# Kernel optimization log

Hardware: AMD Instinct MI355X
Metric: run time of the kernel (lower is better)

The kernel has to match this reference:

```python
import jax, jax.numpy as jnp
import numpy as np

B, N, D, A, E, T, H, O = 2, 2048, 64, 16, 2, 5, 128, 1


def setup_inputs() -> dict:
    key = jax.random.key(0)
    ks = jax.random.split(key, 12)
    s = 0.02  # torch init: normal(0, 0.02), biases zero
    return {
        "prop_state": jax.random.normal(ks[0], (B, N, D), jnp.float32),
        "annotation": jax.random.normal(ks[1], (B, N, A), jnp.float32),
        "adj_mat": jax.random.uniform(ks[2], (B, N, 2 * N * E), jnp.float32),
        "W_in": s * jax.random.normal(ks[3], (E, D, D), jnp.float32),
        "b_in": jnp.zeros((E, D), jnp.float32),
        "W_out": s * jax.random.normal(ks[4], (E, D, D), jnp.float32),
        "b_out": jnp.zeros((E, D), jnp.float32),
        "Wr": s * jax.random.normal(ks[5], (3 * D, D), jnp.float32),
        "br": jnp.zeros((D,), jnp.float32),
        "Wz": s * jax.random.normal(ks[6], (3 * D, D), jnp.float32),
        "bz": jnp.zeros((D,), jnp.float32),
        "Wh": s * jax.random.normal(ks[7], (3 * D, D), jnp.float32),
        "bh": jnp.zeros((D,), jnp.float32),
        "Wo1": s * jax.random.normal(ks[8], (D + A, H), jnp.float32),
        "bo1": jnp.zeros((H,), jnp.float32),
        "Wo2": s * jax.random.normal(ks[9], (H, O), jnp.float32),
        "bo2": jnp.zeros((O,), jnp.float32),
    }


def reference(prop_state, annotation, adj_mat, W_in, b_in, W_out, b_out,
              Wr, br, Wz, bz, Wh, bh, Wo1, bo1, Wo2, bo2):
    Bb, Nn, Dd = prop_state.shape
    Ee = W_in.shape[0]
    A_in = adj_mat[:, :, : Nn * Ee]   # [B, N, E*N]
    A_out = adj_mat[:, :, Nn * Ee :]  # [B, N, E*N]
    h = prop_state
    for _ in range(T):
        # per-edge-type linear maps; edge-type-major flatten (index = e*N + v)
        ins = (jnp.einsum('bnd,edk->benk', h, W_in) + b_in[None, :, None, :]).reshape(Bb, Ee * Nn, Dd)
        outs = (jnp.einsum('bnd,edk->benk', h, W_out) + b_out[None, :, None, :]).reshape(Bb, Ee * Nn, Dd)
        a_in = jnp.einsum('bnm,bmd->bnd', A_in, ins)
        a_out = jnp.einsum('bnm,bmd->bnd', A_out, outs)
        a = jnp.concatenate([a_in, a_out, h], axis=-1)          # [B, N, 3D]
        r = jax.nn.sigmoid(a @ Wr + br)
        z = jax.nn.sigmoid(a @ Wz + bz)
        joint = jnp.concatenate([a_in, a_out, r * h], axis=-1)  # [B, N, 3D]
        h_hat = jnp.tanh(joint @ Wh + bh)
        h = (1.0 - z) * h + z * h_hat
    x = jnp.concatenate([h, annotation], axis=-1)               # [B, N, D+A]
    x = jax.nn.sigmoid(x @ Wo1 + bo1)
    x = x @ Wo2 + bo2                                           # [B, N, O]
    return x.sum(axis=2)                                        # [B, N]
```

## Files before the change

kernel.cpp:

```cpp
#include <hip/hip_runtime.h>
#include <cstdint>
#include <cstddef>

#define B_ 2
#define N_ 2048
#define D_ 64
#define E_ 2
#define T_ 5

typedef short bf16x8 __attribute__((ext_vector_type(8)));
typedef unsigned short u16x8 __attribute__((ext_vector_type(8)));
typedef float f32x16 __attribute__((ext_vector_type(16)));

__device__ __forceinline__ unsigned short f2bf(float f) {
    unsigned int x = __float_as_uint(f);
    x += 0x7FFFu + ((x >> 16) & 1u);
    return (unsigned short)(x >> 16);
}

__global__ void convert_kernel(const float* __restrict__ adj, u16x8* __restrict__ Abf) {
    int rt = blockIdx.x, c = blockIdx.y, bd = blockIdx.z;
    int b = bd >> 1, dir = bd & 1;
    int tid = threadIdx.x;

    __shared__ __align__(16) unsigned short sb[32][520];

    const float* base = adj + ((size_t)(b * N_ + rt * 32)) * (2 * N_ * E_) + dir * (N_ * E_) + c * 512;

    #pragma unroll
    for (int p = 0; p < 4; ++p) {
        int r = p * 8 + (tid >> 5);
        int i = tid & 31;
        const float* rowp = base + (size_t)r * (2 * N_ * E_);
        #pragma unroll
        for (int j = 0; j < 4; ++j) {
            float4 f = *(const float4*)(rowp + i * 4 + j * 128);
            int kl = i * 4 + j * 128;
            sb[r][kl + 0] = f2bf(f.x);
            sb[r][kl + 1] = f2bf(f.y);
            sb[r][kl + 2] = f2bf(f.z);
            sb[r][kl + 3] = f2bf(f.w);
        }
    }
    __syncthreads();

    int l = tid & 63;
    int row = l & 31, khalf = l >> 5;
    int ktl0 = tid >> 6;
    u16x8* dst = Abf + ((size_t)(bd * 64 + rt) * 256 + c * 32 + ktl0) * 64 + l;
    #pragma unroll
    for (int q = 0; q < 8; ++q) {
        int ktl = ktl0 + q * 4;
        u16x8 v = *(const u16x8*)&sb[row][ktl * 16 + khalf * 8];
        dst[(size_t)q * 4 * 64] = v;
    }
}

__global__ void transform_kernel(const float* __restrict__ h,
                                 const float* __restrict__ W_in, const float* __restrict__ b_in,
                                 const float* __restrict__ W_out, const float* __restrict__ b_out,
                                 u16x8* __restrict__ VT) {
    int y = blockIdx.y;
    int e = y & 1, dir = (y >> 1) & 1, b = y >> 2;
    int bd = y >> 1;
    const float* W = (dir ? W_out : W_in) + e * D_ * D_;
    const float* bias = (dir ? b_out : b_in) + e * D_;
    int n0 = blockIdx.x * 64;

    __shared__ float hs[64][65];
    __shared__ float Ws[64][64];
    __shared__ float os[64][65];

    int tid = threadIdx.x;
    #pragma unroll
    for (int i = 0; i < 16; ++i) {
        int idx = tid + 256 * i;
        int r = idx >> 6, c = idx & 63;
        hs[r][c] = h[((size_t)(b * N_ + n0 + r)) * D_ + c];
        Ws[r][c] = W[idx];
    }
    __syncthreads();

    int g = tid >> 6, l = tid & 63;
    float acc[16];
    #pragma unroll
    for (int j = 0; j < 16; ++j) acc[j] = bias[g * 16 + j];
    for (int k = 0; k < 64; ++k) {
        float hv = hs[l][k];
        #pragma unroll
        for (int j = 0; j < 16; ++j) acc[j] = fmaf(hv, Ws[k][g * 16 + j], acc[j]);
    }
    #pragma unroll
    for (int j = 0; j < 16; ++j) os[l][g * 16 + j] = acc[j];
    __syncthreads();

    #pragma unroll
    for (int c = 0; c < 2; ++c) {
        int chunk = tid + 256 * c;
        int kt_local = chunk >> 7;
        int sub = (chunk >> 6) & 1;
        int ln = chunk & 63;
        int d = sub * 32 + (ln & 31);
        int nbase = kt_local * 16 + (ln >> 5) * 8;
        u16x8 o;
        #pragma unroll
        for (int j = 0; j < 8; ++j) o[j] = f2bf(os[nbase + j][d]);
        int ktg = e * 128 + blockIdx.x * 4 + kt_local;
        VT[((size_t)bd * 512 + ktg * 2 + sub) * 64 + ln] = o;
    }
}

__global__ void __launch_bounds__(512, 2) aggregate_kernel(
        const bf16x8* __restrict__ Abf, const bf16x8* __restrict__ VT,
        float* __restrict__ apart) {
    int bx = blockIdx.x;
    int bd = blockIdx.y;
    int sp = blockIdx.z;
    int tid = threadIdx.x;
    int w = tid >> 6, lane = tid & 63;
    int rt = bx * 8 + w;
    int kt0 = sp * 32;

    const bf16x8* Ap = Abf + ((size_t)(bd * 64 + rt) * 256 + kt0) * 64 + lane;
    const bf16x8* Vp = VT + (size_t)bd * 32768 + (size_t)kt0 * 128 + lane;

    f32x16 acc0 = {}, acc1 = {};
    #pragma unroll 4
    for (int kk = 0; kk < 32; ++kk) {
        bf16x8 a  = Ap[(size_t)kk * 64];
        bf16x8 b0 = Vp[(size_t)kk * 128];
        bf16x8 b1 = Vp[(size_t)kk * 128 + 64];
        acc0 = __builtin_amdgcn_mfma_f32_32x32x16_bf16(a, b0, acc0, 0, 0, 0);
        acc1 = __builtin_amdgcn_mfma_f32_32x32x16_bf16(a, b1, acc1, 0, 0, 0);
    }

    float* Cp = apart + ((size_t)(sp * 4 + bd) * 2048) * 64;
    int col = lane & 31;
    int rbase = rt * 32 + 4 * (lane >> 5);
    #pragma unroll
    for (int reg = 0; reg < 16; ++reg) {
        int row = rbase + (reg & 3) + 8 * (reg >> 2);
        Cp[(size_t)row * 64 + col]      = acc0[reg];
        Cp[(size_t)row * 64 + col + 32] = acc1[reg];
    }
}

__global__ void gru_kernel(float* __restrict__ h,
                           const float* __restrict__ apart,
                           const float* __restrict__ Wr, const float* __restrict__ br,
                           const float* __restrict__ Wz, const float* __restrict__ bz,
                           const float* __restrict__ Wh, const float* __restrict__ bh) {
    int tid = threadIdx.x;
    int grp = tid >> 6, d = tid & 63;
    int g = blockIdx.x * 16 + grp;
    int b = g >> 11, n = g & 2047;

    __shared__ float sa[16][3][64];
    float ain = 0.f, aout = 0.f;
    #pragma unroll
    for (int s = 0; s < 8; ++s) {
        ain  += apart[(((size_t)(s * 4 + b * 2    )) * 2048 + n) * 64 + d];
        aout += apart[(((size_t)(s * 4 + b * 2 + 1)) * 2048 + n) * 64 + d];
    }
    float h_d = h[(size_t)g * 64 + d];
    sa[grp][0][d] = ain;
    sa[grp][1][d] = aout;
    sa[grp][2][d] = h_d;
    __syncthreads();

    float accr = br[d], accz = bz[d];
    #pragma unroll 8
    for (int k = 0; k < 64; ++k) {
        float a0 = sa[grp][0][k], a1 = sa[grp][1][k], a2 = sa[grp][2][k];
        accr = fmaf(a0, Wr[k * 64 + d], accr);
        accr = fmaf(a1, Wr[(64 + k) * 64 + d], accr);
        accr = fmaf(a2, Wr[(128 + k) * 64 + d], accr);
        accz = fmaf(a0, Wz[k * 64 + d], accz);
        accz = fmaf(a1, Wz[(64 + k) * 64 + d], accz);
        accz = fmaf(a2, Wz[(128 + k) * 64 + d], accz);
    }
    float r = 1.0f / (1.0f + expf(-accr));
    float z = 1.0f / (1.0f + expf(-accz));

    __syncthreads();
    sa[grp][2][d] = r * h_d;
    __syncthreads();

    float acch = bh[d];
    #pragma unroll 8
    for (int k = 0; k < 64; ++k) {
        float a0 = sa[grp][0][k], a1 = sa[grp][1][k], a2 = sa[grp][2][k];
        acch = fmaf(a0, Wh[k * 64 + d], acch);
        acch = fmaf(a1, Wh[(64 + k) * 64 + d], acch);
        acch = fmaf(a2, Wh[(128 + k) * 64 + d], acch);
    }
    float hh = tanhf(acch);
    h[(size_t)g * 64 + d] = (1.0f - z) * h_d + z * hh;
}

__global__ void output_kernel(const float* __restrict__ h, const float* __restrict__ ann,
                              const float* __restrict__ Wo1, const float* __restrict__ bo1,
                              const float* __restrict__ Wo2, const float* __restrict__ bo2,
                              float* __restrict__ out) {
    int tid = threadIdx.x;
    int grp = tid >> 7, j = tid & 127;
    int g = blockIdx.x * 2 + grp;

    __shared__ float sx[2][80];
    __shared__ float sy[2][128];
    if (j < 64)       sx[grp][j] = h[(size_t)g * 64 + j];
    else if (j < 80)  sx[grp][j] = ann[(size_t)g * 16 + (j - 64)];
    __syncthreads();

    float acc = bo1[j];
    #pragma unroll
    for (int i = 0; i < 80; ++i) acc = fmaf(sx[grp][i], Wo1[i * 128 + j], acc);
    float y = 1.0f / (1.0f + expf(-acc));
    sy[grp][j] = y * Wo2[j];
    __syncthreads();

    if (j == 0) {
        float s = bo2[0];
        #pragma unroll
        for (int k = 0; k < 128; ++k) s += sy[grp][k];
        out[g] = s;
    }
}

extern "C" void kernel_launch(void* const* d_in, const int* in_sizes, int n_in,
                              void* d_out, int out_size, void* d_ws, size_t ws_size,
                              hipStream_t stream) {
    const float* prop = (const float*)d_in[0];
    const float* ann  = (const float*)d_in[1];
    const float* adj  = (const float*)d_in[2];
    const float* W_in = (const float*)d_in[3];
    const float* b_in = (const float*)d_in[4];
    const float* W_out= (const float*)d_in[5];
    const float* b_out= (const float*)d_in[6];
    const float* Wr   = (const float*)d_in[7];
    const float* br   = (const float*)d_in[8];
    const float* Wz   = (const float*)d_in[9];
    const float* bz   = (const float*)d_in[10];
    const float* Wh   = (const float*)d_in[11];
    const float* bh   = (const float*)d_in[12];
    const float* Wo1  = (const float*)d_in[13];
    const float* bo1  = (const float*)d_in[14];
    const float* Wo2  = (const float*)d_in[15];
    const float* bo2  = (const float*)d_in[16];
    float* out = (float*)d_out;

    char* ws = (char*)d_ws;
    u16x8* Abf   = (u16x8*)ws;
    u16x8* VT    = (u16x8*)(ws + (64ull << 20));
    float* apart = (float*)(ws + (66ull << 20));
    float* h     = (float*)(ws + (82ull << 20));

    convert_kernel<<<dim3(64, 8, 4), 256, 0, stream>>>(adj, Abf);
    hipMemcpyAsync(h, prop, (size_t)B_ * N_ * D_ * sizeof(float),
                   hipMemcpyDeviceToDevice, stream);

    for (int t = 0; t < T_; ++t) {
        transform_kernel<<<dim3(32, 8), 256, 0, stream>>>(
            h, W_in, b_in, W_out, b_out, VT);
        aggregate_kernel<<<dim3(8, 4, 8), 512, 0, stream>>>(
            (const bf16x8*)Abf, (const bf16x8*)VT, apart);
        gru_kernel<<<dim3(B_ * N_ / 16), 1024, 0, stream>>>(
            h, apart, Wr, br, Wz, bz, Wh, bh);
    }
    output_kernel<<<dim3(B_ * N_ / 2), 256, 0, stream>>>(
        h, ann, Wo1, bo1, Wo2, bo2, out);
}
```

Baseline: 483.0 us.

## Fuse timestep loop into one persistent cooperative kernel with grid syncs

Replaces the per-timestep transform, aggregate, GRU and output kernel launches with a single cooperative kernel of 256 workgroups that runs all phases and separates them with grid.sync(). Each workgroup keeps its 16 rows of hidden state in shared memory across timesteps, so h no longer round-trips through global memory and the initial device-to-device copy is dropped. This removes about 16 kernel launches and their tail gaps. In exchange it pays grid-wide barrier costs, and the GRU and transform phases now use fewer threads per row.

```diff
diff --git a/kernel.cpp b/kernel.cpp
--- a/kernel.cpp
+++ b/kernel.cpp
@@ -1,6 +1,9 @@
 #include <hip/hip_runtime.h>
+#include <hip/hip_cooperative_groups.h>
 #include <cstdint>
 #include <cstddef>
+
+namespace cg = cooperative_groups;
 
 #define B_ 2
 #define N_ 2048
@@ -56,71 +59,55 @@
     }
 }
 
-__global__ void transform_kernel(const float* __restrict__ h,
-                                 const float* __restrict__ W_in, const float* __restrict__ b_in,
-                                 const float* __restrict__ W_out, const float* __restrict__ b_out,
-                                 u16x8* __restrict__ VT) {
-    int y = blockIdx.y;
-    int e = y & 1, dir = (y >> 1) & 1, b = y >> 2;
-    int bd = y >> 1;
-    const float* W = (dir ? W_out : W_in) + e * D_ * D_;
+struct SM {
+    float hs[16][64];
+    float os[4][16][66];
+    float sa[16][3][64];
+    float red[4][2];
+};
+
+__device__ __forceinline__ void transform_emit(
+        SM* sm, u16x8* VT,
+        const float* W_in, const float* b_in,
+        const float* W_out, const float* b_out,
+        int b, int ktgl, int tid)
+{
+    int u = tid >> 6, lane = tid & 63;
+    int dir = u & 1, e = (u >> 1) & 1, nh = u >> 2;
+    const float* W    = (dir ? W_out : W_in) + e * D_ * D_;
     const float* bias = (dir ? b_out : b_in) + e * D_;
-    int n0 = blockIdx.x * 64;
-
-    __shared__ float hs[64][65];
-    __shared__ float Ws[64][64];
-    __shared__ float os[64][65];
-
-    int tid = threadIdx.x;
-    #pragma unroll
-    for (int i = 0; i < 16; ++i) {
-        int idx = tid + 256 * i;
-        int r = idx >> 6, c = idx & 63;
-        hs[r][c] = h[((size_t)(b * N_ + n0 + r)) * D_ + c];
-        Ws[r][c] = W[idx];
-    }
-    __syncthreads();
-
-    int g = tid >> 6, l = tid & 63;
-    float acc[16];
-    #pragma unroll
-    for (int j = 0; j < 16; ++j) acc[j] = bias[g * 16 + j];
+    int d = lane;
+    float acc[8];
+    #pragma unroll
+    for (int i = 0; i < 8; ++i) acc[i] = bias[d];
     for (int k = 0; k < 64; ++k) {
-        float hv = hs[l][k];
-        #pragma unroll
-        for (int j = 0; j < 16; ++j) acc[j] = fmaf(hv, Ws[k][g * 16 + j], acc[j]);
-    }
-    #pragma unroll
-    for (int j = 0; j < 16; ++j) os[l][g * 16 + j] = acc[j];
-    __syncthreads();
-
-    #pragma unroll
-    for (int c = 0; c < 2; ++c) {
-        int chunk = tid + 256 * c;
-        int kt_local = chunk >> 7;
-        int sub = (chunk >> 6) & 1;
-        int ln = chunk & 63;
-        int d = sub * 32 + (ln & 31);
-        int nbase = kt_local * 16 + (ln >> 5) * 8;
-        u16x8 o;
-        #pragma unroll
-        for (int j = 0; j < 8; ++j) o[j] = f2bf(os[nbase + j][d]);
-        int ktg = e * 128 + blockIdx.x * 4 + kt_local;
-        VT[((size_t)bd * 512 + ktg * 2 + sub) * 64 + ln] = o;
-    }
-}
-
-__global__ void __launch_bounds__(512, 2) aggregate_kernel(
-        const bf16x8* __restrict__ Abf, const bf16x8* __restrict__ VT,
-        float* __restrict__ apart) {
-    int bx = blockIdx.x;
-    int bd = blockIdx.y;
-    int sp = blockIdx.z;
-    int tid = threadIdx.x;
+        float wv = W[k * 64 + d];
+        #pragma unroll
+        for (int i = 0; i < 8; ++i) acc[i] = fmaf(sm->hs[nh * 8 + i][k], wv, acc[i]);
+    }
+    int de = dir * 2 + e;
+    #pragma unroll
+    for (int i = 0; i < 8; ++i) sm->os[de][nh * 8 + i][d] = acc[i];
+    __syncthreads();
+
+    int sub = u >> 2;
+    int dd = sub * 32 + (lane & 31);
+    int nb = (lane >> 5) * 8;
+    u16x8 o;
+    #pragma unroll
+    for (int j = 0; j < 8; ++j) o[j] = f2bf(sm->os[de][nb + j][dd]);
+    int bd = b * 2 + dir;
+    int ktg = e * 128 + ktgl;
+    VT[((size_t)bd * 512 + ktg * 2 + sub) * 64 + lane] = o;
+}
+
+__device__ __forceinline__ void aggregate_phase(
+        const bf16x8* Abf, const bf16x8* VT, float* apart, int wg, int tid)
+{
+    int rb = wg & 7, bd = (wg >> 3) & 3, sp = wg >> 5;
     int w = tid >> 6, lane = tid & 63;
-    int rt = bx * 8 + w;
+    int rt = rb * 8 + w;
     int kt0 = sp * 32;
-
     const bf16x8* Ap = Abf + ((size_t)(bd * 64 + rt) * 256 + kt0) * 64 + lane;
     const bf16x8* Vp = VT + (size_t)bd * 32768 + (size_t)kt0 * 128 + lane;
 
@@ -133,7 +120,6 @@
         acc0 = __builtin_amdgcn_mfma_f32_32x32x16_bf16(a, b0, acc0, 0, 0, 0);
         acc1 = __builtin_amdgcn_mfma_f32_32x32x16_bf16(a, b1, acc1, 0, 0, 0);
     }
-
     float* Cp = apart + ((size_t)(sp * 4 + bd) * 2048) * 64;
     int col = lane & 31;
     int rbase = rt * 32 + 4 * (lane >> 5);
@@ -145,86 +131,121 @@
     }
 }
 
-__global__ void gru_kernel(float* __restrict__ h,
-                           const float* __restrict__ apart,
-                           const float* __restrict__ Wr, const float* __restrict__ br,
-                           const float* __restrict__ Wz, const float* __restrict__ bz,
-                           const float* __restrict__ Wh, const float* __restrict__ bh) {
-    int tid = threadIdx.x;
-    int grp = tid >> 6, d = tid & 63;
-    int g = blockIdx.x * 16 + grp;
-    int b = g >> 11, n = g & 2047;
-
-    __shared__ float sa[16][3][64];
-    float ain = 0.f, aout = 0.f;
-    #pragma unroll
-    for (int s = 0; s < 8; ++s) {
-        ain  += apart[(((size_t)(s * 4 + b * 2    )) * 2048 + n) * 64 + d];
-        aout += apart[(((size_t)(s * 4 + b * 2 + 1)) * 2048 + n) * 64 + d];
-    }
-    float h_d = h[(size_t)g * 64 + d];
-    sa[grp][0][d] = ain;
-    sa[grp][1][d] = aout;
-    sa[grp][2][d] = h_d;
-    __syncthreads();
-
-    float accr = br[d], accz = bz[d];
-    #pragma unroll 8
-    for (int k = 0; k < 64; ++k) {
-        float a0 = sa[grp][0][k], a1 = sa[grp][1][k], a2 = sa[grp][2][k];
-        accr = fmaf(a0, Wr[k * 64 + d], accr);
-        accr = fmaf(a1, Wr[(64 + k) * 64 + d], accr);
-        accr = fmaf(a2, Wr[(128 + k) * 64 + d], accr);
-        accz = fmaf(a0, Wz[k * 64 + d], accz);
-        accz = fmaf(a1, Wz[(64 + k) * 64 + d], accz);
-        accz = fmaf(a2, Wz[(128 + k) * 64 + d], accz);
-    }
-    float r = 1.0f / (1.0f + expf(-accr));
-    float z = 1.0f / (1.0f + expf(-accz));
-
-    __syncthreads();
-    sa[grp][2][d] = r * h_d;
-    __syncthreads();
-
-    float acch = bh[d];
-    #pragma unroll 8
-    for (int k = 0; k < 64; ++k) {
-        float a0 = sa[grp][0][k], a1 = sa[grp][1][k], a2 = sa[grp][2][k];
-        acch = fmaf(a0, Wh[k * 64 + d], acch);
-        acch = fmaf(a1, Wh[(64 + k) * 64 + d], acch);
-        acch = fmaf(a2, Wh[(128 + k) * 64 + d], acch);
-    }
-    float hh = tanhf(acch);
-    h[(size_t)g * 64 + d] = (1.0f - z) * h_d + z * hh;
-}
-
-__global__ void output_kernel(const float* __restrict__ h, const float* __restrict__ ann,
-                              const float* __restrict__ Wo1, const float* __restrict__ bo1,
-                              const float* __restrict__ Wo2, const float* __restrict__ bo2,
-                              float* __restrict__ out) {
-    int tid = threadIdx.x;
-    int grp = tid >> 7, j = tid & 127;
-    int g = blockIdx.x * 2 + grp;
-
-    __shared__ float sx[2][80];
-    __shared__ float sy[2][128];
-    if (j < 64)       sx[grp][j] = h[(size_t)g * 64 + j];
-    else if (j < 80)  sx[grp][j] = ann[(size_t)g * 16 + (j - 64)];
-    __syncthreads();
-
-    float acc = bo1[j];
-    #pragma unroll
-    for (int i = 0; i < 80; ++i) acc = fmaf(sx[grp][i], Wo1[i * 128 + j], acc);
-    float y = 1.0f / (1.0f + expf(-acc));
-    sy[grp][j] = y * Wo2[j];
-    __syncthreads();
-
-    if (j == 0) {
-        float s = bo2[0];
-        #pragma unroll
-        for (int k = 0; k < 128; ++k) s += sy[grp][k];
-        out[g] = s;
-    }
+__device__ __forceinline__ void gru_phase(
+        SM* sm, const float* apart,
+        const float* Wr, const float* br, const float* Wz, const float* bz,
+        const float* Wh, const float* bh, int b, int n0, int tid)
+{
+    int u = tid >> 6, d = tid & 63;
+    #pragma unroll
+    for (int s = 0; s < 2; ++s) {
+        int nl = u * 2 + s;
+        int n = n0 + nl;
+        float ain = 0.f, aout = 0.f;
+        #pragma unroll
+        for (int sp = 0; sp < 8; ++sp) {
+            ain  += apart[(((size_t)(sp * 4 + b * 2    )) * 2048 + n) * 64 + d];
+            aout += apart[(((size_t)(sp * 4 + b * 2 + 1)) * 2048 + n) * 64 + d];
+        }
+        float h_d = sm->hs[nl][d];
+        sm->sa[nl][0][d] = ain;
+        sm->sa[nl][1][d] = aout;
+        sm->sa[nl][2][d] = h_d;
+        float accr = br[d], accz = bz[d];
+        #pragma unroll 8
+        for (int k = 0; k < 64; ++k) {
+            float a0 = sm->sa[nl][0][k], a1 = sm->sa[nl][1][k], a2 = sm->sa[nl][2][k];
+            accr = fmaf(a0, Wr[k * 64 + d], accr);
+            accr = fmaf(a1, Wr[(64 + k) * 64 + d], accr);
+            accr = fmaf(a2, Wr[(128 + k) * 64 + d], accr);
+            accz = fmaf(a0, Wz[k * 64 + d], accz);
+            accz = fmaf(a1, Wz[(64 + k) * 64 + d], accz);
+            accz = fmaf(a2, Wz[(128 + k) * 64 + d], accz);
+        }
+        float r = 1.0f / (1.0f + expf(-accr));
+        float z = 1.0f / (1.0f + expf(-accz));
+        sm->sa[nl][2][d] = r * h_d;
+        float acch = bh[d];
+        #pragma unroll 8
+        for (int k = 0; k < 64; ++k) {
+            float a0 = sm->sa[nl][0][k], a1 = sm->sa[nl][1][k], a2 = sm->sa[nl][2][k];
+            acch = fmaf(a0, Wh[k * 64 + d], acch);
+            acch = fmaf(a1, Wh[(64 + k) * 64 + d], acch);
+            acch = fmaf(a2, Wh[(128 + k) * 64 + d], acch);
+        }
+        float hh = tanhf(acch);
+        sm->hs[nl][d] = (1.0f - z) * h_d + z * hh;
+    }
+}
+
+__device__ __forceinline__ void output_phase(
+        SM* sm, const float* ann,
+        const float* Wo1, const float* bo1, const float* Wo2, const float* bo2,
+        float* out, int g0, int tid)
+{
+    int sub = tid >> 7, j = tid & 127;
+    int wv = (tid >> 6) & 1;
+    #pragma unroll
+    for (int s = 0; s < 4; ++s) {
+        int nl = sub * 4 + s;
+        int g = g0 + nl;
+        float acc = bo1[j];
+        #pragma unroll
+        for (int i = 0; i < 64; ++i) acc = fmaf(sm->hs[nl][i], Wo1[i * 128 + j], acc);
+        #pragma unroll
+        for (int i = 0; i < 16; ++i) acc = fmaf(ann[(size_t)g * 16 + i], Wo1[(64 + i) * 128 + j], acc);
+        float y = 1.0f / (1.0f + expf(-acc));
+        float v = y * Wo2[j];
+        #pragma unroll
+        for (int off = 32; off > 0; off >>= 1) v += __shfl_down(v, off, 64);
+        if ((tid & 63) == 0) sm->red[sub][wv] = v;
+        __syncthreads();
+        if (j == 0) out[g] = sm->red[sub][0] + sm->red[sub][1] + bo2[0];
+        __syncthreads();
+    }
+}
+
+__global__ void __launch_bounds__(512, 1) ggnn_coop(
+        const float* prop, const float* ann,
+        const bf16x8* Abf, u16x8* VT, float* apart,
+        const float* W_in, const float* b_in,
+        const float* W_out, const float* b_out,
+        const float* Wr, const float* br,
+        const float* Wz, const float* bz,
+        const float* Wh, const float* bh,
+        const float* Wo1, const float* bo1,
+        const float* Wo2, const float* bo2,
+        float* out)
+{
+    cg::grid_group grid = cg::this_grid();
+    __shared__ SM sm;
+    int wg = blockIdx.x, tid = threadIdx.x;
+    int g0 = wg * 16;
+    int b = g0 >> 11;
+    int n0 = g0 & 2047;
+    int ktgl = n0 >> 4;
+
+    #pragma unroll
+    for (int i = 0; i < 2; ++i) {
+        int idx = tid + i * 512;
+        sm.hs[idx >> 6][idx & 63] = prop[(size_t)g0 * 64 + idx];
+    }
+    __syncthreads();
+    transform_emit(&sm, VT, W_in, b_in, W_out, b_out, b, ktgl, tid);
+    grid.sync();
+
+    for (int t = 0; t < T_; ++t) {
+        aggregate_phase(Abf, (const bf16x8*)VT, apart, wg, tid);
+        grid.sync();
+        gru_phase(&sm, apart, Wr, br, Wz, bz, Wh, bh, b, n0, tid);
+        __syncthreads();
+        if (t < T_ - 1) {
+            transform_emit(&sm, VT, W_in, b_in, W_out, b_out, b, ktgl, tid);
+            grid.sync();
+        }
+    }
+    __syncthreads();
+    output_phase(&sm, ann, Wo1, bo1, Wo2, bo2, out, g0, tid);
 }
 
 extern "C" void kernel_launch(void* const* d_in, const int* in_sizes, int n_in,
@@ -250,23 +271,19 @@
     float* out = (float*)d_out;
 
     char* ws = (char*)d_ws;
-    u16x8* Abf   = (u16x8*)ws;
-    u16x8* VT    = (u16x8*)(ws + (64ull << 20));
-    float* apart = (float*)(ws + (66ull << 20));
-    float* h     = (float*)(ws + (82ull << 20));
+    u16x8* Abf    = (u16x8*)ws;
+    u16x8* VT     = (u16x8*)(ws + (64ull << 20));
+    float* apart  = (float*)(ws + (66ull << 20));
 
     convert_kernel<<<dim3(64, 8, 4), 256, 0, stream>>>(adj, Abf);
-    hipMemcpyAsync(h, prop, (size_t)B_ * N_ * D_ * sizeof(float),
-                   hipMemcpyDeviceToDevice, stream);
-
-    for (int t = 0; t < T_; ++t) {
-        transform_kernel<<<dim3(32, 8), 256, 0, stream>>>(
-            h, W_in, b_in, W_out, b_out, VT);
-        aggregate_kernel<<<dim3(8, 4, 8), 512, 0, stream>>>(
-            (const bf16x8*)Abf, (const bf16x8*)VT, apart);
-        gru_kernel<<<dim3(B_ * N_ / 16), 1024, 0, stream>>>(
-            h, apart, Wr, br, Wz, bz, Wh, bh);
-    }
-    output_kernel<<<dim3(B_ * N_ / 2), 256, 0, stream>>>(
-        h, ann, Wo1, bo1, Wo2, bo2, out);
-}
+
+    const bf16x8* Abf_c = (const bf16x8*)Abf;
+    void* args[] = {
+        (void*)&prop, (void*)&ann, (void*)&Abf_c, (void*)&VT, (void*)&apart,
+        (void*)&W_in, (void*)&b_in, (void*)&W_out, (void*)&b_out,
+        (void*)&Wr, (void*)&br, (void*)&Wz, (void*)&bz, (void*)&Wh, (void*)&bh,
+        (void*)&Wo1, (void*)&bo1, (void*)&Wo2, (void*)&bo2, (void*)&out
+    };
+    hipLaunchCooperativeKernel((void*)ggnn_coop, dim3(256), dim3(512),
+                               args, 0, stream);
+}
```

Measured after the change: 818.0 us. 69.3% more time.

## Fuse edge transforms into GRU kernel and output MLP into last GRU step

Applied to the files above, without the earlier changes.

The per-step transform kernel is merged into the end of the GRU kernel. After updating h for its 16 nodes, each block computes the four edge-type/direction linear maps and writes the bf16 VT tiles for the next aggregation. The final GRU step also computes the output MLP, using wave shuffles for the reduction, and the initial device-to-device copy is replaced by running the transform directly on prop_state. The aim is to cut kernel launches and the round trip of h through global memory. In exchange, intra-wave barriers are dropped, which relies on each 64-thread group being exactly one wavefront.

```diff
diff --git a/kernel.cpp b/kernel.cpp
--- a/kernel.cpp
+++ b/kernel.cpp
@@ -56,10 +56,10 @@
     }
 }
 
-__global__ void transform_kernel(const float* __restrict__ h,
-                                 const float* __restrict__ W_in, const float* __restrict__ b_in,
-                                 const float* __restrict__ W_out, const float* __restrict__ b_out,
-                                 u16x8* __restrict__ VT) {
+__global__ void transform0_kernel(const float* __restrict__ h,
+                                  const float* __restrict__ W_in, const float* __restrict__ b_in,
+                                  const float* __restrict__ W_out, const float* __restrict__ b_out,
+                                  u16x8* __restrict__ VT) {
     int y = blockIdx.y;
     int e = y & 1, dir = (y >> 1) & 1, b = y >> 2;
     int bd = y >> 1;
@@ -145,33 +145,30 @@
     }
 }
 
-__global__ void gru_kernel(float* __restrict__ h,
-                           const float* __restrict__ apart,
-                           const float* __restrict__ Wr, const float* __restrict__ br,
-                           const float* __restrict__ Wz, const float* __restrict__ bz,
-                           const float* __restrict__ Wh, const float* __restrict__ bh) {
-    int tid = threadIdx.x;
-    int grp = tid >> 6, d = tid & 63;
-    int g = blockIdx.x * 16 + grp;
-    int b = g >> 11, n = g & 2047;
-
-    __shared__ float sa[16][3][64];
+__device__ __forceinline__ void gru_core(
+        const float* __restrict__ h_in, const float* __restrict__ apart,
+        const float* __restrict__ Wr, const float* __restrict__ br,
+        const float* __restrict__ Wz, const float* __restrict__ bz,
+        const float* __restrict__ Wh, const float* __restrict__ bh,
+        float sa[16][3][64], float hs[16][64],
+        int b, int n0, int g0, int tid)
+{
+    int nl = tid >> 6, d = tid & 63;
+    int n = n0 + nl;
     float ain = 0.f, aout = 0.f;
     #pragma unroll
-    for (int s = 0; s < 8; ++s) {
-        ain  += apart[(((size_t)(s * 4 + b * 2    )) * 2048 + n) * 64 + d];
-        aout += apart[(((size_t)(s * 4 + b * 2 + 1)) * 2048 + n) * 64 + d];
-    }
-    float h_d = h[(size_t)g * 64 + d];
-    sa[grp][0][d] = ain;
-    sa[grp][1][d] = aout;
-    sa[grp][2][d] = h_d;
-    __syncthreads();
-
+    for (int sp = 0; sp < 8; ++sp) {
+        ain  += apart[(((size_t)(sp * 4 + b * 2    )) * 2048 + n) * 64 + d];
+        aout += apart[(((size_t)(sp * 4 + b * 2 + 1)) * 2048 + n) * 64 + d];
+    }
+    float h_d = h_in[((size_t)g0 + nl) * 64 + d];
+    sa[nl][0][d] = ain;
+    sa[nl][1][d] = aout;
+    sa[nl][2][d] = h_d;
     float accr = br[d], accz = bz[d];
     #pragma unroll 8
     for (int k = 0; k < 64; ++k) {
-        float a0 = sa[grp][0][k], a1 = sa[grp][1][k], a2 = sa[grp][2][k];
+        float a0 = sa[nl][0][k], a1 = sa[nl][1][k], a2 = sa[nl][2][k];
         accr = fmaf(a0, Wr[k * 64 + d], accr);
         accr = fmaf(a1, Wr[(64 + k) * 64 + d], accr);
         accr = fmaf(a2, Wr[(128 + k) * 64 + d], accr);
@@ -181,49 +178,124 @@
     }
     float r = 1.0f / (1.0f + expf(-accr));
     float z = 1.0f / (1.0f + expf(-accz));
-
-    __syncthreads();
-    sa[grp][2][d] = r * h_d;
-    __syncthreads();
-
+    sa[nl][2][d] = r * h_d;
     float acch = bh[d];
     #pragma unroll 8
     for (int k = 0; k < 64; ++k) {
-        float a0 = sa[grp][0][k], a1 = sa[grp][1][k], a2 = sa[grp][2][k];
+        float a0 = sa[nl][0][k], a1 = sa[nl][1][k], a2 = sa[nl][2][k];
         acch = fmaf(a0, Wh[k * 64 + d], acch);
         acch = fmaf(a1, Wh[(64 + k) * 64 + d], acch);
         acch = fmaf(a2, Wh[(128 + k) * 64 + d], acch);
     }
     float hh = tanhf(acch);
-    h[(size_t)g * 64 + d] = (1.0f - z) * h_d + z * hh;
-}
-
-__global__ void output_kernel(const float* __restrict__ h, const float* __restrict__ ann,
-                              const float* __restrict__ Wo1, const float* __restrict__ bo1,
-                              const float* __restrict__ Wo2, const float* __restrict__ bo2,
-                              float* __restrict__ out) {
-    int tid = threadIdx.x;
-    int grp = tid >> 7, j = tid & 127;
-    int g = blockIdx.x * 2 + grp;
-
-    __shared__ float sx[2][80];
-    __shared__ float sy[2][128];
-    if (j < 64)       sx[grp][j] = h[(size_t)g * 64 + j];
-    else if (j < 80)  sx[grp][j] = ann[(size_t)g * 16 + (j - 64)];
-    __syncthreads();
-
-    float acc = bo1[j];
-    #pragma unroll
-    for (int i = 0; i < 80; ++i) acc = fmaf(sx[grp][i], Wo1[i * 128 + j], acc);
-    float y = 1.0f / (1.0f + expf(-acc));
-    sy[grp][j] = y * Wo2[j];
-    __syncthreads();
-
+    hs[nl][d] = (1.0f - z) * h_d + z * hh;
+}
+
+__global__ void __launch_bounds__(1024, 1) gru_mid_kernel(
+        const float* __restrict__ h_in, float* __restrict__ h_out,
+        const float* __restrict__ apart,
+        const float* __restrict__ Wr, const float* __restrict__ br,
+        const float* __restrict__ Wz, const float* __restrict__ bz,
+        const float* __restrict__ Wh, const float* __restrict__ bh,
+        const float* __restrict__ W_in, const float* __restrict__ b_in,
+        const float* __restrict__ W_out, const float* __restrict__ b_out,
+        u16x8* __restrict__ VT)
+{
+    __shared__ float sa[16][3][64];
+    __shared__ float hs[16][64];
+    __shared__ float os[4][16][66];
+
+    int wg = blockIdx.x, tid = threadIdx.x;
+    int g0 = wg * 16;
+    int b = g0 >> 11, n0 = g0 & 2047;
+    int ktgl = n0 >> 4;
+
+    gru_core(h_in, apart, Wr, br, Wz, bz, Wh, bh, sa, hs, b, n0, g0, tid);
+
+    {
+        int nl = tid >> 6, d = tid & 63;
+        h_out[((size_t)g0 + nl) * 64 + d] = hs[nl][d];
+    }
+    __syncthreads();
+
+    int u = tid >> 6, lane = tid & 63;
+    {
+        int de = u & 3, q = u >> 2;
+        int dir = de >> 1, e = de & 1;
+        const float* W    = (dir ? W_out : W_in) + e * D_ * D_;
+        const float* bias = (dir ? b_out : b_in) + e * D_;
+        int d = lane;
+        float acc[4];
+        #pragma unroll
+        for (int i = 0; i < 4; ++i) acc[i] = bias[d];
+        for (int k = 0; k < 64; ++k) {
+            float wv = W[k * 64 + d];
+            #pragma unroll
+            for (int i = 0; i < 4; ++i) acc[i] = fmaf(hs[q * 4 + i][k], wv, acc[i]);
+        }
+        #pragma unroll
+        for (int i = 0; i < 4; ++i) os[de][q * 4 + i][d] = acc[i];
+    }
+    __syncthreads();
+
+    if (u < 8) {
+        int de = u >> 1, sub = u & 1;
+        int dir = de >> 1, e = de & 1;
+        int dd = sub * 32 + (lane & 31);
+        int nb = (lane >> 5) * 8;
+        u16x8 o;
+        #pragma unroll
+        for (int j = 0; j < 8; ++j) o[j] = f2bf(os[de][nb + j][dd]);
+        int bd = b * 2 + dir;
+        int ktg = e * 128 + ktgl;
+        VT[((size_t)bd * 512 + ktg * 2 + sub) * 64 + lane] = o;
+    }
+}
+
+__global__ void __launch_bounds__(1024, 1) gru_last_kernel(
+        const float* __restrict__ h_in,
+        const float* __restrict__ apart,
+        const float* __restrict__ Wr, const float* __restrict__ br,
+        const float* __restrict__ Wz, const float* __restrict__ bz,
+        const float* __restrict__ Wh, const float* __restrict__ bh,
+        const float* __restrict__ ann,
+        const float* __restrict__ Wo1, const float* __restrict__ bo1,
+        const float* __restrict__ Wo2, const float* __restrict__ bo2,
+        float* __restrict__ out)
+{
+    __shared__ float sa[16][3][64];
+    __shared__ float hs[16][64];
+    __shared__ float red[8][2][2];
+
+    int wg = blockIdx.x, tid = threadIdx.x;
+    int g0 = wg * 16;
+    int b = g0 >> 11, n0 = g0 & 2047;
+
+    gru_core(h_in, apart, Wr, br, Wz, bz, Wh, bh, sa, hs, b, n0, g0, tid);
+    __syncthreads();
+
+    int sub = tid >> 7, j = tid & 127;
+    int wv = (tid >> 6) & 1;
+    #pragma unroll
+    for (int s = 0; s < 2; ++s) {
+        int nl = sub * 2 + s;
+        int g = g0 + nl;
+        float acc = bo1[j];
+        #pragma unroll
+        for (int i = 0; i < 64; ++i) acc = fmaf(hs[nl][i], Wo1[i * 128 + j], acc);
+        #pragma unroll
+        for (int i = 0; i < 16; ++i) acc = fmaf(ann[(size_t)g * 16 + i], Wo1[(64 + i) * 128 + j], acc);
+        float y = 1.0f / (1.0f + expf(-acc));
+        float v = y * Wo2[j];
+        #pragma unroll
+        for (int off = 32; off > 0; off >>= 1) v += __shfl_down(v, off, 64);
+        if ((tid & 63) == 0) red[sub][wv][s] = v;
+    }
+    __syncthreads();
     if (j == 0) {
-        float s = bo2[0];
-        #pragma unroll
-        for (int k = 0; k < 128; ++k) s += sy[grp][k];
-        out[g] = s;
+        #pragma unroll
+        for (int s = 0; s < 2; ++s)
+            out[g0 + sub * 2 + s] = red[sub][0][s] + red[sub][1][s] + bo2[0];
     }
 }
 
@@ -250,23 +322,27 @@
     float* out = (float*)d_out;
 
     char* ws = (char*)d_ws;
-    u16x8* Abf   = (u16x8*)ws;
-    u16x8* VT    = (u16x8*)(ws + (64ull << 20));
-    float* apart = (float*)(ws + (66ull << 20));
-    float* h     = (float*)(ws + (82ull << 20));
+    u16x8* Abf    = (u16x8*)ws;
+    u16x8* VT     = (u16x8*)(ws + (64ull << 20));
+    float* apart  = (float*)(ws + (66ull << 20));
+    float* h      = (float*)(ws + (82ull << 20));
 
     convert_kernel<<<dim3(64, 8, 4), 256, 0, stream>>>(adj, Abf);
-    hipMemcpyAsync(h, prop, (size_t)B_ * N_ * D_ * sizeof(float),
-                   hipMemcpyDeviceToDevice, stream);
+    transform0_kernel<<<dim3(32, 8), 256, 0, stream>>>(
+        prop, W_in, b_in, W_out, b_out, VT);
 
     for (int t = 0; t < T_; ++t) {
-        transform_kernel<<<dim3(32, 8), 256, 0, stream>>>(
-            h, W_in, b_in, W_out, b_out, VT);
         aggregate_kernel<<<dim3(8, 4, 8), 512, 0, stream>>>(
             (const bf16x8*)Abf, (const bf16x8*)VT, apart);
-        gru_kernel<<<dim3(B_ * N_ / 16), 1024, 0, stream>>>(
-            h, apart, Wr, br, Wz, bz, Wh, bh);
-    }
-    output_kernel<<<dim3(B_ * N_ / 2), 256, 0, stream>>>(
-        h, ann, Wo1, bo1, Wo2, bo2, out);
-}
+        const float* h_in = (t == 0) ? prop : h;
+        if (t < T_ - 1) {
+            gru_mid_kernel<<<dim3(256), 1024, 0, stream>>>(
+                h_in, h, apart, Wr, br, Wz, bz, Wh, bh,
+                W_in, b_in, W_out, b_out, VT);
+        } else {
+            gru_last_kernel<<<dim3(256), 1024, 0, stream>>>(
+                h_in, apart, Wr, br, Wz, bz, Wh, bh,
+                ann, Wo1, bo1, Wo2, bo2, out);
+        }
+    }
+}
```

Measured after the change: 490.7 us. About the same (+1.6%).
